# Performance work log

Hardware: AMD Instinct MI355X
Metric: run time of the kernel (lower is better)

The kernel has to match this reference:

```python
import jax, jax.numpy as jnp
import numpy as np

HEADS = 16
DIM_HEAD = 64
SCALE = DIM_HEAD ** -0.5


def setup_inputs() -> dict:
    key = jax.random.key(0)
    k1, k2, k3, k4 = jax.random.split(key, 4)
    b, n, dim = 2, 2048, 1024
    inner = HEADS * DIM_HEAD  # 1024
    return {
        "x": jax.random.normal(k1, (b, n, dim), dtype=jnp.float32),
        "x1": jax.random.normal(k2, (b, n, dim), dtype=jnp.float32),
        "W_qkv": jax.random.normal(k3, (dim, inner * 3), dtype=jnp.float32) * (dim ** -0.5),
        "W_out": jax.random.normal(k4, (inner, dim), dtype=jnp.float32) * (inner ** -0.5),
        "b_out": jnp.zeros((dim,), dtype=jnp.float32),
    }


def _split_heads(t):
    b, n, hd = t.shape
    return t.reshape(b, n, HEADS, DIM_HEAD).transpose(0, 2, 1, 3)  # b h n d


def _merge_heads(t):
    b, h, n, d = t.shape
    return t.transpose(0, 2, 1, 3).reshape(b, n, h * d)


def reference(x, x1, W_qkv, W_out, b_out):
    qkv = jnp.split(x @ W_qkv, 3, axis=-1)
    qkv1 = jnp.split(x1 @ W_qkv, 3, axis=-1)
    q, k, v = map(_split_heads, qkv)
    q1, k1, v1 = map(_split_heads, qkv1)

    # cross attention: x queries attend to x1 keys/values, and vice versa
    attn = jax.nn.softmax(jnp.einsum('bhnd,bhmd->bhnm', q, k1) * SCALE, axis=-1)
    attn1 = jax.nn.softmax(jnp.einsum('bhnd,bhmd->bhnm', q1, k) * SCALE, axis=-1)
    out = _merge_heads(jnp.einsum('bhnm,bhmd->bhnd', attn, v1))
    out1 = _merge_heads(jnp.einsum('bhnm,bhmd->bhnd', attn1, v))

    out = out @ W_out + b_out
    out1 = out1 @ W_out + b_out
    return out, out1
```

## Files before the change

### kernel.cpp

```cpp
#include <hip/hip_runtime.h>
#include <hip/hip_bf16.h>


typedef __attribute__((ext_vector_type(8))) short short8;
typedef __attribute__((ext_vector_type(4))) float f32x4;
typedef __attribute__((ext_vector_type(16))) float f32x16;

#define MFMA_BF16(a, b, c) __builtin_amdgcn_mfma_f32_16x16x32_bf16((a), (b), (c), 0, 0, 0)
#define MFMA32(a, b, c)    __builtin_amdgcn_mfma_f32_32x32x16_bf16((a), (b), (c), 0, 0, 0)

__device__ __forceinline__ ushort f2bf(float f) {
    __hip_bfloat16 h = __float2bfloat16(f);
    return *reinterpret_cast<ushort*>(&h);
}

__device__ __forceinline__ unsigned cvtpk(float lo, float hi) {
    unsigned r;
    asm("v_cvt_pk_bf16_f32 %0, %1, %2" : "=v"(r) : "v"(lo), "v"(hi));
    return r;
}

__device__ __forceinline__ void gload_lds16(const void* g, void* l) {
    __builtin_amdgcn_global_load_lds(
        (const __attribute__((address_space(1))) void*)g,
        (__attribute__((address_space(3))) void*)l, 16, 0, 0);
}

__global__ __launch_bounds__(256) void prep_k(const float* __restrict__ x,
                                              const float* __restrict__ x1,
                                              ushort* __restrict__ xb,
                                              const float* __restrict__ wqkv,
                                              ushort* __restrict__ wqkv_t,
                                              const float* __restrict__ wout,
                                              ushort* __restrict__ wout_t) {
    __shared__ ushort tile[32][33];
    const int b = blockIdx.x;
    if (b < 8192) {
        const int idx = b * 256 + threadIdx.x;
        const int half = 1048576;
        const float* src = (idx < half) ? x : x1;
        const int i = (idx < half ? idx : idx - half) * 4;
        float4 v = *(const float4*)(src + i);
        ushort4 o;
        o.x = f2bf(v.x); o.y = f2bf(v.y); o.z = f2bf(v.z); o.w = f2bf(v.w);
        *(ushort4*)(xb + (size_t)idx * 4) = o;
        return;
    }
    const int id = b - 8192;
    int bx = id & 127;
    const int by = id >> 7;
    const float* in; ushort* out; int C;
    if (bx < 96) { in = wqkv; out = wqkv_t; C = 3072; }
    else         { bx -= 96; in = wout; out = wout_t; C = 1024; }
    const int R = 1024;
    const int c0 = bx * 32, r0 = by * 32;
    const int tx = threadIdx.x & 31, ty = threadIdx.x >> 5;
#pragma unroll
    for (int i = 0; i < 4; ++i)
        tile[ty * 4 + i][tx] = f2bf(in[(size_t)(r0 + ty * 4 + i) * C + c0 + tx]);
    __syncthreads();
#pragma unroll
    for (int i = 0; i < 4; ++i)
        out[(size_t)(c0 + ty * 4 + i) * R + r0 + tx] = tile[tx][ty * 4 + i];
}

__global__ __launch_bounds__(256) void qkv_gemm(const ushort* __restrict__ xb,
                                                const ushort* __restrict__ wt,
                                                ushort* __restrict__ qb,
                                                ushort* __restrict__ kb,
                                                ushort* __restrict__ vb) {
    __shared__ __align__(16) ushort As[128 * 64];
    __shared__ __align__(16) ushort Bs[128 * 64];

    const int n0 = blockIdx.x * 128;
    const int m0 = blockIdx.y * 128;
    const int t = threadIdx.x;
    const int lane = t & 63, w = t >> 6;
    const int wm = (w >> 1) * 64, wn = (w & 1) * 64;
    const int l16 = lane & 15, lq = lane >> 4;

    const int srow = lane >> 3;
    const int scol = ((lane & 7) * 16) ^ (srow << 4);

    f32x4 acc[4][4] = {};

    for (int k0 = 0; k0 < 1024; k0 += 64) {
        __syncthreads();
#pragma unroll
        for (int c = 0; c < 4; ++c) {
            const int ch = w * 4 + c;
            const int row = ch * 8 + srow;
            gload_lds16((const char*)xb + ((size_t)(m0 + row) * 1024 + k0) * 2 + scol,
                        (char*)As + ch * 1024);
            gload_lds16((const char*)wt + ((size_t)(n0 + row) * 1024 + k0) * 2 + scol,
                        (char*)Bs + ch * 1024);
        }
        __syncthreads();
#pragma unroll
        for (int kc = 0; kc < 2; ++kc) {
            short8 a[4], b[4];
#pragma unroll
            for (int i = 0; i < 4; ++i) {
                const int row = wm + i * 16 + l16;
                a[i] = *(const short8*)((const char*)As + row * 128 +
                                        ((kc * 64 + lq * 16) ^ ((row & 7) << 4)));
            }
#pragma unroll
            for (int j = 0; j < 4; ++j) {
                const int row = wn + j * 16 + l16;
                b[j] = *(const short8*)((const char*)Bs + row * 128 +
                                        ((kc * 64 + lq * 16) ^ ((row & 7) << 4)));
            }
#pragma unroll
            for (int i = 0; i < 4; ++i)
#pragma unroll
                for (int j = 0; j < 4; ++j) acc[i][j] = MFMA_BF16(a[i], b[j], acc[i][j]);
        }
    }

    const int which = (n0 >> 10);
    const float qscale = (which == 0) ? 0.125f : 1.0f;

#pragma unroll
    for (int i = 0; i < 4; ++i) {
#pragma unroll
        for (int jj = 0; jj < 4; ++jj) {
#pragma unroll
            for (int rr = 0; rr < 4; ++rr) {
                const int m = m0 + wm + i * 16 + lq * 4 + rr;
                const int nc = n0 + wn + jj * 16 + l16;
                const ushort bv = f2bf(acc[i][jj][rr] * qscale);
                const int s = m >> 12;
                const int mm = m & 4095;
                const int rem = nc & 1023;
                const int h = rem >> 6, d = rem & 63;
                const int sb = (s << 1) | (mm >> 11);
                const int pos = mm & 2047;
                const size_t bh = (size_t)(sb * 16 + h);
                if (which == 0)      qb[(bh * 2048 + pos) * 64 + d] = bv;
                else if (which == 1) kb[(bh * 2048 + pos) * 64 + d] = bv;
                else                 vb[(bh * 64 + d) * 2048 + pos] = bv;
            }
        }
    }
}

__global__ __launch_bounds__(256, 4) void attn_k(const ushort* __restrict__ qb,
                                                 const ushort* __restrict__ kb,
                                                 const ushort* __restrict__ vb,
                                                 ushort* __restrict__ ob) {
    __shared__ __align__(16) ushort Ks[2][4096];
    __shared__ __align__(16) ushort Vs[2][4096];

    const int t = threadIdx.x, lane = t & 63, w = t >> 6;
    const int l31 = lane & 31, hi = lane >> 5;

    const int lid = blockIdx.x;
    const int xcd = lid & 7, kk = lid >> 3;
    const int qt = kk & 15;
    const int g = xcd + ((kk >> 4) << 3);
    const int h = g & 15, sb = g >> 4;
    const int s = sb >> 1, bb = sb & 1;
    const int kvsb = ((1 - s) << 1) | bb;
    const int q0 = qt * 128 + w * 32;

    const ushort* qp = qb + (size_t)(sb * 16 + h) * 2048 * 64;
    const char* kp = (const char*)(kb + (size_t)(kvsb * 16 + h) * 2048 * 64);
    const char* vp = (const char*)(vb + (size_t)(kvsb * 16 + h) * 64 * 2048);

    short8 qf[4];
#pragma unroll
    for (int c = 0; c < 4; ++c)
        qf[c] = *(const short8*)(qp + (size_t)(q0 + l31) * 64 + c * 16 + hi * 8);

    f32x16 o0 = {}, o1 = {};
    float lsum = 0.f;

    const int swl = ((lane >> 3) & 7) << 4;
    auto stage = [&](int buf, int key0) {
#pragma unroll
        for (int i = 0; i < 2; ++i) {
            const int ch = w * 2 + i;
            const int off = ch * 1024 + lane * 16;
            gload_lds16(kp + (size_t)key0 * 128 + (off ^ swl),
                        (char*)&Ks[buf][0] + ch * 1024);
            const int rd = ch * 8 + (lane >> 3);
            const int cb = (lane & 7) * 16;
            gload_lds16(vp + (size_t)rd * 4096 + (size_t)key0 * 2 + (cb ^ swl),
                        (char*)&Vs[buf][0] + ch * 1024);
        }
    };

    stage(0, 0);
    __syncthreads();

    for (int tt = 0; tt < 32; ++tt) {
        const int cur = tt & 1;
        if (tt < 31) stage(cur ^ 1, (tt + 1) * 64);

        const char* Kc = (const char*)&Ks[cur][0];
        const char* Vc = (const char*)&Vs[cur][0];
        const int sw = (l31 & 7) << 4;

        f32x16 scA = {}, scB = {};
        __builtin_amdgcn_s_setprio(1);
#pragma unroll
        for (int c = 0; c < 4; ++c) {
            const int off = c * 32 + hi * 16;
            short8 ka = *(const short8*)(Kc + l31 * 128 + (off ^ sw));
            short8 kb2 = *(const short8*)(Kc + (32 + l31) * 128 + (off ^ sw));
            scA = MFMA32(ka, qf[c], scA);
            scB = MFMA32(kb2, qf[c], scB);
        }
        __builtin_amdgcn_s_setprio(0);

#pragma unroll
        for (int r = 0; r < 16; ++r) scA[r] = __expf(scA[r]);
#pragma unroll
        for (int r = 0; r < 16; ++r) scB[r] = __expf(scB[r]);
        {
            float sA = (((scA[0] + scA[1]) + (scA[2] + scA[3])) +
                        ((scA[4] + scA[5]) + (scA[6] + scA[7]))) +
                       (((scA[8] + scA[9]) + (scA[10] + scA[11])) +
                        ((scA[12] + scA[13]) + (scA[14] + scA[15])));
            float sB = (((scB[0] + scB[1]) + (scB[2] + scB[3])) +
                        ((scB[4] + scB[5]) + (scB[6] + scB[7]))) +
                       (((scB[8] + scB[9]) + (scB[10] + scB[11])) +
                        ((scB[12] + scB[13]) + (scB[14] + scB[15])));
            lsum += sA + sB;
        }

        __builtin_amdgcn_s_setprio(1);
#define PACK_PV(P, BASE, KS)                                                     \
        {                                                                        \
            unsigned R00 = cvtpk(P[BASE + 0], P[BASE + 1]);                      \
            unsigned R10 = cvtpk(P[BASE + 2], P[BASE + 3]);                      \
            unsigned R01 = cvtpk(P[BASE + 4], P[BASE + 5]);                      \
            unsigned R11 = cvtpk(P[BASE + 6], P[BASE + 7]);                      \
            unsigned ra = (unsigned)__shfl_xor((int)(hi ? R00 : R01), 32);       \
            unsigned rb = (unsigned)__shfl_xor((int)(hi ? R10 : R11), 32);       \
            union { unsigned u[4]; short8 s8; } ap;                              \
            ap.u[0] = hi ? ra : R00;                                             \
            ap.u[1] = hi ? rb : R10;                                             \
            ap.u[2] = hi ? R01 : ra;                                             \
            ap.u[3] = hi ? R11 : rb;                                             \
            const int vo = (KS) * 32 + hi * 16;                                  \
            short8 v0 = *(const short8*)(Vc + l31 * 128 + (vo ^ sw));            \
            short8 v1 = *(const short8*)(Vc + (32 + l31) * 128 + (vo ^ sw));     \
            o0 = MFMA32(ap.s8, v0, o0);                                          \
            o1 = MFMA32(ap.s8, v1, o1);                                          \
        }
        PACK_PV(scA, 0, 0)
        PACK_PV(scA, 8, 1)
        PACK_PV(scB, 0, 2)
        PACK_PV(scB, 8, 3)
#undef PACK_PV
        __builtin_amdgcn_s_setprio(0);

        __syncthreads();
    }

    const float lf = lsum + __shfl_xor(lsum, 32);
    const size_t obase = (size_t)(sb * 2048 + q0) * 1024 + h * 64 + l31;
#pragma unroll
    for (int r = 0; r < 16; ++r) {
        const int qrow = (r & 3) + 8 * (r >> 2) + 4 * hi;
        const float invl = 1.f / __shfl(lf, qrow);
        ob[obase + (size_t)qrow * 1024]      = f2bf(o0[r] * invl);
        ob[obase + (size_t)qrow * 1024 + 32] = f2bf(o1[r] * invl);
    }
}

__global__ __launch_bounds__(256) void out_gemm(const ushort* __restrict__ ob,
                                                const ushort* __restrict__ wot,
                                                const float* __restrict__ bias,
                                                float* __restrict__ out) {
    __shared__ __align__(16) ushort As[128 * 64];
    __shared__ __align__(16) ushort Bs[128 * 64];

    const int n0 = blockIdx.x * 128;
    const int m0 = blockIdx.y * 128;
    const int t = threadIdx.x;
    const int lane = t & 63, w = t >> 6;
    const int wm = (w >> 1) * 64, wn = (w & 1) * 64;
    const int l16 = lane & 15, lq = lane >> 4;

    const int srow = lane >> 3;
    const int scol = ((lane & 7) * 16) ^ (srow << 4);

    f32x4 acc[4][4] = {};

    for (int k0 = 0; k0 < 1024; k0 += 64) {
        __syncthreads();
#pragma unroll
        for (int c = 0; c < 4; ++c) {
            const int ch = w * 4 + c;
            const int row = ch * 8 + srow;
            gload_lds16((const char*)ob + ((size_t)(m0 + row) * 1024 + k0) * 2 + scol,
                        (char*)As + ch * 1024);
            gload_lds16((const char*)wot + ((size_t)(n0 + row) * 1024 + k0) * 2 + scol,
                        (char*)Bs + ch * 1024);
        }
        __syncthreads();
#pragma unroll
        for (int kc = 0; kc < 2; ++kc) {
            short8 a[4], b[4];
#pragma unroll
            for (int i = 0; i < 4; ++i) {
                const int row = wm + i * 16 + l16;
                a[i] = *(const short8*)((const char*)As + row * 128 +
                                        ((kc * 64 + lq * 16) ^ ((row & 7) << 4)));
            }
#pragma unroll
            for (int j = 0; j < 4; ++j) {
                const int row = wn + j * 16 + l16;
                b[j] = *(const short8*)((const char*)Bs + row * 128 +
                                        ((kc * 64 + lq * 16) ^ ((row & 7) << 4)));
            }
#pragma unroll
            for (int i = 0; i < 4; ++i)
#pragma unroll
                for (int j = 0; j < 4; ++j) acc[i][j] = MFMA_BF16(a[i], b[j], acc[i][j]);
        }
    }

    float biasf[4];
#pragma unroll
    for (int jj = 0; jj < 4; ++jj) biasf[jj] = bias[n0 + wn + jj * 16 + l16];

#pragma unroll
    for (int i = 0; i < 4; ++i)
#pragma unroll
        for (int jj = 0; jj < 4; ++jj)
#pragma unroll
            for (int rr = 0; rr < 4; ++rr) {
                const int m = m0 + wm + i * 16 + lq * 4 + rr;
                const int nc = n0 + wn + jj * 16 + l16;
                out[(size_t)m * 1024 + nc] = acc[i][jj][rr] + biasf[jj];
            }
}

extern "C" void kernel_launch(void* const* d_in, const int* in_sizes, int n_in,
                              void* d_out, int out_size, void* d_ws, size_t ws_size,
                              hipStream_t stream) {
    (void)out_size; (void)ws_size;
    const float *x = nullptr, *x1 = nullptr, *wqkv = nullptr, *wout = nullptr, *bias = nullptr;
    for (int i = 0; i < n_in; ++i) {
        const int sz = in_sizes[i];
        const float* p = (const float*)d_in[i];
        if (sz == 4194304)      { if (!x) x = p; else x1 = p; }
        else if (sz == 3145728) wqkv = p;
        else if (sz == 1048576) wout = p;
        else if (sz == 1024)    bias = p;
    }
    float* out = (float*)d_out;

    ushort* ws      = (ushort*)d_ws;
    ushort* wqkv_t  = ws;
    ushort* wout_t  = wqkv_t + 3072 * 1024;
    ushort* xb      = wout_t + 1024 * 1024;
    ushort* qbuf    = xb + 8388608;
    ushort* kbuf    = qbuf + 8388608;
    ushort* vbuf    = kbuf + 8388608;
    ushort* obuf    = xb;

    prep_k<<<12288, 256, 0, stream>>>(x, x1, xb, wqkv, wqkv_t, wout, wout_t);
    qkv_gemm<<<dim3(24, 64), 256, 0, stream>>>(xb, wqkv_t, qbuf, kbuf, vbuf);
    attn_k<<<1024, 256, 0, stream>>>(qbuf, kbuf, vbuf, obuf);
    out_gemm<<<dim3(8, 64), 256, 0, stream>>>(obuf, wout_t, bias, out);
}
```

Baseline: 302.2 us.

## Permute K rows to drop P shuffles and stage V transpose through LDS

The attention kernel now loads K rows in a permuted lane order. This makes the MFMA score output layout line up directly with the A-operand layout needed for the PV product, so the cross-half lane shuffles and selects are removed from the inner loop. Separately, the QKV GEMM writes its V output by transposing the tile through shared memory and storing 16-byte vectors, instead of scattered 2-byte strided stores. The trade-off is an extra LDS round trip and barrier in the V-writing blocks, and the correctness of the permutation depends on the MFMA register layout.

```diff
diff --git a/kernel.cpp b/kernel.cpp
--- a/kernel.cpp
+++ b/kernel.cpp
@@ -69,8 +69,9 @@
                                                 ushort* __restrict__ qb,
                                                 ushort* __restrict__ kb,
                                                 ushort* __restrict__ vb) {
-    __shared__ __align__(16) ushort As[128 * 64];
-    __shared__ __align__(16) ushort Bs[128 * 64];
+    __shared__ __align__(16) ushort Sm[2][128 * 64];
+    ushort* As = &Sm[0][0];
+    ushort* Bs = &Sm[1][0];
 
     const int n0 = blockIdx.x * 128;
     const int m0 = blockIdx.y * 128;
@@ -119,8 +120,38 @@
     }
 
     const int which = (n0 >> 10);
+
+    if (which == 2) {
+        __syncthreads();
+        char* Cs = (char*)&Sm[0][0];
+#pragma unroll
+        for (int i = 0; i < 4; ++i)
+#pragma unroll
+            for (int jj = 0; jj < 4; ++jj) {
+                const int ncl = wn + jj * 16 + l16;
+                const int mb  = (wm + i * 16 + lq * 4) * 2;
+                uint2 pk;
+                pk.x = cvtpk(acc[i][jj][0], acc[i][jj][1]);
+                pk.y = cvtpk(acc[i][jj][2], acc[i][jj][3]);
+                *(uint2*)(Cs + ncl * 256 + (mb ^ ((ncl & 7) << 4))) = pk;
+            }
+        asm volatile("s_waitcnt lgkmcnt(0)" ::: "memory");
+#pragma unroll
+        for (int it = 0; it < 8; ++it) {
+            const int r  = wn + it * 8 + (lane >> 3);
+            const int cb = wm * 2 + (lane & 7) * 16;
+            short8 v = *(const short8*)(Cs + r * 256 + (cb ^ ((r & 7) << 4)));
+            const int rem = (n0 + r) & 1023;
+            const int hh = rem >> 6, d = rem & 63;
+            const int m = m0 + wm + (lane & 7) * 8;
+            const int ss = m >> 12, mm = m & 4095;
+            const int sbv = (ss << 1) | (mm >> 11), pos = mm & 2047;
+            *(short8*)(vb + ((size_t)(sbv * 16 + hh) * 64 + d) * 2048 + pos) = v;
+        }
+        return;
+    }
+
     const float qscale = (which == 0) ? 0.125f : 1.0f;
-
 #pragma unroll
     for (int i = 0; i < 4; ++i) {
 #pragma unroll
@@ -137,9 +168,8 @@
                 const int sb = (s << 1) | (mm >> 11);
                 const int pos = mm & 2047;
                 const size_t bh = (size_t)(sb * 16 + h);
-                if (which == 0)      qb[(bh * 2048 + pos) * 64 + d] = bv;
-                else if (which == 1) kb[(bh * 2048 + pos) * 64 + d] = bv;
-                else                 vb[(bh * 64 + d) * 2048 + pos] = bv;
+                if (which == 0) qb[(bh * 2048 + pos) * 64 + d] = bv;
+                else            kb[(bh * 2048 + pos) * 64 + d] = bv;
             }
         }
     }
@@ -194,21 +224,24 @@
     stage(0, 0);
     __syncthreads();
 
+    const int pl = (l31 & ~12) | ((l31 & 4) << 1) | ((l31 & 8) >> 1);
+    const int swp = (pl & 7) << 4;
+    const int swv = (l31 & 7) << 4;
+
     for (int tt = 0; tt < 32; ++tt) {
         const int cur = tt & 1;
         if (tt < 31) stage(cur ^ 1, (tt + 1) * 64);
 
         const char* Kc = (const char*)&Ks[cur][0];
         const char* Vc = (const char*)&Vs[cur][0];
-        const int sw = (l31 & 7) << 4;
 
         f32x16 scA = {}, scB = {};
         __builtin_amdgcn_s_setprio(1);
 #pragma unroll
         for (int c = 0; c < 4; ++c) {
             const int off = c * 32 + hi * 16;
-            short8 ka = *(const short8*)(Kc + l31 * 128 + (off ^ sw));
-            short8 kb2 = *(const short8*)(Kc + (32 + l31) * 128 + (off ^ sw));
+            short8 ka  = *(const short8*)(Kc + pl * 128 + (off ^ swp));
+            short8 kb2 = *(const short8*)(Kc + (32 + pl) * 128 + (off ^ swp));
             scA = MFMA32(ka, qf[c], scA);
             scB = MFMA32(kb2, qf[c], scB);
         }
@@ -233,20 +266,14 @@
         __builtin_amdgcn_s_setprio(1);
 #define PACK_PV(P, BASE, KS)                                                     \
         {                                                                        \
-            unsigned R00 = cvtpk(P[BASE + 0], P[BASE + 1]);                      \
-            unsigned R10 = cvtpk(P[BASE + 2], P[BASE + 3]);                      \
-            unsigned R01 = cvtpk(P[BASE + 4], P[BASE + 5]);                      \
-            unsigned R11 = cvtpk(P[BASE + 6], P[BASE + 7]);                      \
-            unsigned ra = (unsigned)__shfl_xor((int)(hi ? R00 : R01), 32);       \
-            unsigned rb = (unsigned)__shfl_xor((int)(hi ? R10 : R11), 32);       \
             union { unsigned u[4]; short8 s8; } ap;                              \
-            ap.u[0] = hi ? ra : R00;                                             \
-            ap.u[1] = hi ? rb : R10;                                             \
-            ap.u[2] = hi ? R01 : ra;                                             \
-            ap.u[3] = hi ? R11 : rb;                                             \
+            ap.u[0] = cvtpk(P[BASE + 0], P[BASE + 1]);                           \
+            ap.u[1] = cvtpk(P[BASE + 2], P[BASE + 3]);                           \
+            ap.u[2] = cvtpk(P[BASE + 4], P[BASE + 5]);                           \
+            ap.u[3] = cvtpk(P[BASE + 6], P[BASE + 7]);                           \
             const int vo = (KS) * 32 + hi * 16;                                  \
-            short8 v0 = *(const short8*)(Vc + l31 * 128 + (vo ^ sw));            \
-            short8 v1 = *(const short8*)(Vc + (32 + l31) * 128 + (vo ^ sw));     \
+            short8 v0 = *(const short8*)(Vc + l31 * 128 + (vo ^ swv));           \
+            short8 v1 = *(const short8*)(Vc + (32 + l31) * 128 + (vo ^ swv));    \
             o0 = MFMA32(ap.s8, v0, o0);                                          \
             o1 = MFMA32(ap.s8, v1, o1);                                          \
         }
```

After: 279.2 us. 1.08x faster.
